# Performance work log

Hardware: AMD Instinct MI355X
Metric: run time of the kernel (lower is better)

The kernel has to match this reference:

```python
import jax, jax.numpy as jnp
import numpy as np
from jax import lax

N, C, H, W, Q, HD = 2, 64, 96, 96, 147456, 128

def make_coord(h, w):
    # pixel-center coords in [-1,1]; channel 0 -> H dim, channel 1 -> W dim
    y = -1.0 + (2.0 * jnp.arange(h) + 1.0) / h
    x = -1.0 + (2.0 * jnp.arange(w) + 1.0) / w
    yy, xx = jnp.meshgrid(y, x, indexing='ij')
    return jnp.stack([yy, xx], 0)[None]  # [1,2,h,w]

def _pix(c, n):
    # align_corners=False unnormalization
    return ((c + 1.0) * n - 1.0) / 2.0

def gather_nearest(img, cy, cx):
    # img [n,c,h,w]; cy,cx [n,q] in [-1,1] -> [n,q,c]
    n, c, h, w = img.shape
    iy = jnp.clip(jnp.round(_pix(cy, h)).astype(jnp.int32), 0, h - 1)
    ix = jnp.clip(jnp.round(_pix(cx, w)).astype(jnp.int32), 0, w - 1)
    flat = img.reshape(n, c, h * w)
    out = jnp.take_along_axis(flat, (iy * w + ix)[:, None, :], axis=2)
    return out.transpose(0, 2, 1)

def sample_bilinear_border(img, cy, cx):
    # grid_sample bilinear, padding_mode='border', align_corners=False
    n, c, h, w = img.shape
    fy = jnp.clip(_pix(cy, h), 0.0, h - 1.0)
    fx = jnp.clip(_pix(cx, w), 0.0, w - 1.0)
    y0 = jnp.floor(fy); x0 = jnp.floor(fx)
    wy = fy - y0; wx = fx - x0
    y0i = jnp.clip(y0.astype(jnp.int32), 0, h - 1); y1i = jnp.clip(y0i + 1, 0, h - 1)
    x0i = jnp.clip(x0.astype(jnp.int32), 0, w - 1); x1i = jnp.clip(x0i + 1, 0, w - 1)
    flat = img.reshape(n, c, h * w)
    def g(iy, ix):
        return jnp.take_along_axis(flat, (iy * w + ix)[:, None, :], axis=2)
    v = (g(y0i, x0i) * ((1 - wy) * (1 - wx))[:, None, :]
         + g(y0i, x1i) * ((1 - wy) * wx)[:, None, :]
         + g(y1i, x0i) * (wy * (1 - wx))[:, None, :]
         + g(y1i, x1i) * (wy * wx)[:, None, :])
    return v.transpose(0, 2, 1)

def mlp3(x, w1, b1, w2, b2, w3, b3):
    hdd = jax.nn.relu(x @ w1 + b1)
    hdd = jax.nn.relu(hdd @ w2 + b2)
    return hdd @ w3 + b3

def posenc(rel, hd):
    # sinusoid PE: 2 coord dims x (sin,cos) x hd//4 octave bands -> hd feats
    f = (2.0 ** jnp.arange(hd // 4)) * jnp.pi
    ang = rel[..., None] * f  # [n,q,2,hd//4]
    n, q = rel.shape[:2]
    return jnp.concatenate([jnp.sin(ang), jnp.cos(ang)], -1).reshape(n, q, hd)

def reference(lr, feat, raw_disp, coord, cell, coef_w, coef_b, freq_w, freq_b, phase_w,
              im_w1, im_b1, im_w2, im_b2, im_w3, im_b3,
              dp_w1, dp_b1, dp_w2, dp_b2, dp_w3, dp_b3):
    n, c, h, w = feat.shape
    hd = coef_b.shape[0]
    conv = lambda x, wk, bk: lax.conv_general_dilated(
        x, wk, (1, 1), 'SAME', dimension_numbers=('NCHW', 'OIHW', 'NCHW')) + bk[None, :, None, None]
    coef = conv(feat, coef_w, coef_b)
    freq = conv(feat, freq_w, freq_b)
    scale = 2.0 / (cell + 1e-6)[:, 0, 1] / w  # [n]
    disp = raw_disp * scale[:, None, None, None]
    mean_d = jnp.mean(disp, (1, 2, 3), keepdims=True)
    std_d = jnp.std(disp, (1, 2, 3), keepdims=True, ddof=1) + 1e-6
    dnorm = (disp - mean_d) / std_d
    rx, ry = 1.0 / h, 1.0 / w  # 2/dim/2
    fcoord = jnp.broadcast_to(make_coord(h, w), (n, 2, h, w))
    hw = jnp.array([h, w], coord.dtype)
    phase = (cell * hw) @ phase_w  # [n,q,hd]
    preds, pdisps, areas = [], [], []
    for vx in (-1, 1):
        for vy in (-1, 1):
            cy = jnp.clip(coord[:, :, 0] + vx * rx + 1e-6, -1 + 1e-6, 1 - 1e-6)
            cx = jnp.clip(coord[:, :, 1] + vy * ry + 1e-6, -1 + 1e-6, 1 - 1e-6)
            q_disp = gather_nearest(dnorm, cy, cx)   # [n,q,1]
            q_inp = gather_nearest(feat, cy, cx)     # [n,q,c]
            q_coef = gather_nearest(coef, cy, cx)    # [n,q,hd]
            q_freq = gather_nearest(freq, cy, cx)    # [n,q,hd]
            q_coord = gather_nearest(fcoord, cy, cx) # [n,q,2]
            rel = (coord - q_coord) * hw
            coord_ff = posenc(rel, hd)
            pdisps.append(mlp3(jnp.concatenate([q_disp, q_inp, rel], -1),
                               dp_w1, dp_b1, dp_w2, dp_b2, dp_w3, dp_b3))
            qf = q_freq * coord_ff + phase
            preds.append(mlp3(q_coef * qf, im_w1, im_b1, im_w2, im_b2, im_w3, im_b3))
            areas.append(jnp.abs(rel[:, :, 0] * rel[:, :, 1]) + 1e-9)
    tot = areas[0] + areas[1] + areas[2] + areas[3]
    order = [3, 2, 1, 0]  # local-ensemble diagonal area swap
    ret = sum(preds[i] * (areas[order[i]] / tot)[..., None] for i in range(4))
    ret_d = sum(pdisps[i] * (areas[order[i]] / tot)[..., None] for i in range(4))
    cy, cx = coord[:, :, 0], coord[:, :, 1]
    rgb = ret + sample_bilinear_border(lr, cy, cx)
    out_disp = ret_d + sample_bilinear_border(disp, cy, cx)
    return jnp.concatenate([rgb, out_disp], -1)  # [n,q,4]

def setup_inputs() -> dict:
    key = jax.random.key(0)
    ks = jax.random.split(key, 16)
    s = 0.02
    return {
        'lr': jax.random.uniform(ks[0], (N, 3, H, W), jnp.float32),
        'feat': jax.random.normal(ks[1], (N, C, H, W), jnp.float32),
        'raw_disp': jax.random.normal(ks[2], (N, 1, H, W), jnp.float32),
        'coord': jax.random.uniform(ks[3], (N, Q, 2), jnp.float32) * 2.0 - 1.0,
        'cell': jnp.full((N, Q, 2), 2.0 / 384.0, jnp.float32),
        'coef_w': jax.random.normal(ks[4], (HD, C, 3, 3), jnp.float32) * s,
        'coef_b': jnp.zeros((HD,), jnp.float32),
        'freq_w': jax.random.normal(ks[5], (HD, C, 3, 3), jnp.float32) * s,
        'freq_b': jnp.zeros((HD,), jnp.float32),
        'phase_w': jax.random.normal(ks[6], (2, HD), jnp.float32) * s,
        'im_w1': jax.random.normal(ks[7], (HD, 256), jnp.float32) * s,
        'im_b1': jnp.zeros((256,), jnp.float32),
        'im_w2': jax.random.normal(ks[8], (256, 256), jnp.float32) * s,
        'im_b2': jnp.zeros((256,), jnp.float32),
        'im_w3': jax.random.normal(ks[9], (256, 3), jnp.float32) * s,
        'im_b3': jnp.zeros((3,), jnp.float32),
        'dp_w1': jax.random.normal(ks[10], (C + 3, 256), jnp.float32) * s,
        'dp_b1': jnp.zeros((256,), jnp.float32),
        'dp_w2': jax.random.normal(ks[11], (256, 256), jnp.float32) * s,
        'dp_b2': jnp.zeros((256,), jnp.float32),
        'dp_w3': jax.random.normal(ks[12], (256, 1), jnp.float32) * s,
        'dp_b3': jnp.zeros((1,), jnp.float32),
    }
```

## Files before the change

kernel.cpp:

```cpp
#include <hip/hip_runtime.h>

#define QTOT 147456

typedef __attribute__((ext_vector_type(8))) short bf16x8;
typedef __attribute__((ext_vector_type(8))) unsigned short u16x8;
typedef __attribute__((ext_vector_type(4))) float f32x4;

union V8 { u16x8 v; unsigned short us[8]; };

__device__ __forceinline__ unsigned short f2b(float f){
  unsigned int u = __float_as_uint(f);
  return (unsigned short)((u + 0x7fffu + ((u >> 16) & 1u)) >> 16);
}
__device__ __forceinline__ float b2f(unsigned short s){
  return __uint_as_float(((unsigned int)s) << 16);
}

#define OFF_STATS   0
#define OFF_FPAD    256
#define OFF_SAMP    (OFF_FPAD + 2458624)
#define OFF_DNORM   (OFF_SAMP + 589824)
#define OFF_COEFT   (OFF_DNORM + 73728)
#define OFF_FREQT   (OFF_COEFT + 4718592)
#define OFF_WIM1    (OFF_FREQT + 4718592)
#define OFF_WIM2    (OFF_WIM1 + 65536)
#define OFF_WIM3    (OFF_WIM2 + 131072)
#define OFF_WDP1    (OFF_WIM3 + 8192)
#define OFF_WDP2    (OFF_WDP1 + 49152)
#define OFF_WDP3    (OFF_WDP2 + 131072)
#define OFF_WCV     (OFF_WDP3 + 8192)

__global__ void kStats(const float* __restrict__ raw_disp, const float* __restrict__ cell,
                       float* __restrict__ stats){
  int n = blockIdx.x;
  float cellv = cell[((size_t)n*QTOT)*2 + 1];
  float scale = 2.0f/(cellv + 1e-6f)/96.0f;
  __shared__ double sd[256], sq[256];
  double s=0.0, s2=0.0;
  for(int i=threadIdx.x;i<9216;i+=256){
    float d = raw_disp[(size_t)n*9216 + i]*scale;
    double dd = (double)d; s += dd; s2 += dd*dd;
  }
  sd[threadIdx.x]=s; sq[threadIdx.x]=s2; __syncthreads();
  for(int o=128;o>0;o>>=1){
    if(threadIdx.x<o){ sd[threadIdx.x]+=sd[threadIdx.x+o]; sq[threadIdx.x]+=sq[threadIdx.x+o]; }
    __syncthreads();
  }
  if(threadIdx.x==0){
    double mean = sd[0]/9216.0;
    double var  = (sq[0] - sd[0]*sd[0]/9216.0)/9215.0;
    if(var < 0.0) var = 0.0;
    stats[n*2+0] = (float)mean;
    stats[n*2+1] = (float)sqrt(var) + 1e-6f;
  }
}

__global__ void kPackImgs(const float* __restrict__ feat, const float* __restrict__ lr,
                          const float* __restrict__ raw_disp, const float* __restrict__ cell,
                          const float* __restrict__ stats,
                          unsigned short* __restrict__ featPad, float* __restrict__ sampT,
                          float* __restrict__ dnormT){
  int i = blockIdx.x*256 + threadIdx.x;
  if(i >= 2*98*98) return;
  int n = i/(98*98); int remi = i%(98*98);
  int py = remi/98, px = remi%98;
  bool inter = (py>=1 && py<=96 && px>=1 && px<=96);
  int y = py-1, x = px-1;
  for(int cb=0;cb<8;cb++){
    V8 v;
    #pragma unroll
    for(int e=0;e<8;e++){
      int c = cb*8+e;
      float f = inter ? feat[(((size_t)n*64 + c)*96 + y)*96 + x] : 0.0f;
      v.us[e] = f2b(f);
    }
    *(u16x8*)(featPad + (size_t)i*64 + cb*8) = v.v;
  }
  if(inter){
    float cellv = cell[((size_t)n*QTOT)*2 + 1];
    float scale = 2.0f/(cellv + 1e-6f)/96.0f;
    float d = raw_disp[((size_t)n*96 + y)*96 + x]*scale;
    size_t p = (size_t)n*9216 + y*96 + x;
    float4 sv;
    sv.x = lr[(((size_t)n*3 + 0)*96 + y)*96 + x];
    sv.y = lr[(((size_t)n*3 + 1)*96 + y)*96 + x];
    sv.z = lr[(((size_t)n*3 + 2)*96 + y)*96 + x];
    sv.w = d;
    *(float4*)(sampT + p*4) = sv;
    dnormT[p] = (d - stats[n*2+0]) / stats[n*2+1];
  }
}

__device__ __forceinline__ void packKN(unsigned short* dst, const float* src,
                                       int K, int N, int Npad, int i){
  int j = i & 7; int tt = i >> 3;
  int col = tt % Npad; tt /= Npad;
  int qq = tt & 3; int kc = tt >> 2;
  int k = kc*32 + qq*8 + j;
  float v = (k < K && col < N) ? src[(size_t)k*N + col] : 0.0f;
  dst[i] = f2b(v);
}

__global__ void kPackW(const float* im_w1, const float* im_w2, const float* im_w3,
                       const float* dp_w1, const float* dp_w2, const float* dp_w3,
                       const float* coef_w, const float* freq_w,
                       unsigned short* wIm1, unsigned short* wIm2, unsigned short* wIm3,
                       unsigned short* wDp1, unsigned short* wDp2, unsigned short* wDp3,
                       unsigned short* wCv){
  int i = blockIdx.x*256 + threadIdx.x;
  if(i < 32768){ packKN(wIm1, im_w1, 128, 256, 256, i); return; } i -= 32768;
  if(i < 65536){ packKN(wIm2, im_w2, 256, 256, 256, i); return; } i -= 65536;
  if(i < 4096){  packKN(wIm3, im_w3, 256, 3, 16, i);    return; } i -= 4096;
  if(i < 24576){ packKN(wDp1, dp_w1, 67, 256, 256, i);  return; } i -= 24576;
  if(i < 65536){ packKN(wDp2, dp_w2, 256, 256, 256, i); return; } i -= 65536;
  if(i < 4096){  packKN(wDp3, dp_w3, 256, 1, 16, i);    return; } i -= 4096;
  if(i < 147456){
    int ii = i;
    int j = ii & 7; int tt = ii >> 3;
    int col = tt % 128; tt /= 128;
    int qq = tt & 3; tt >>= 2;
    int kc = tt & 1; tt >>= 1;
    int tap = tt % 9; int z = tt / 9;
    int k = kc*32 + qq*8 + j;
    const float* w = z ? freq_w : coef_w;
    wCv[i] = f2b(w[((size_t)col*64 + k)*9 + tap]);
  }
}

__global__ __launch_bounds__(512) void kConv(const unsigned short* __restrict__ featPad,
                                             const unsigned short* __restrict__ wCv,
                                             const float* __restrict__ coef_b,
                                             const float* __restrict__ freq_b,
                                             unsigned short* __restrict__ coefT,
                                             unsigned short* __restrict__ freqT){
  int bx = blockIdx.x;
  int y  = blockIdx.y;
  int nz = blockIdx.z; int n = nz >> 1, z = nz & 1;
  const unsigned short* wp = wCv + (size_t)z*73728;
  const float* bias = z ? freq_b : coef_b;
  unsigned short* dst = z ? freqT : coefT;
  int t = threadIdx.x, lane = t & 63, w = t >> 6;
  int x0 = bx*48;
  int colBase = w*16 + (lane & 15);
  int qq = lane >> 4;
  f32x4 acc[3] = {};
  #pragma unroll
  for(int tap=0;tap<9;tap++){
    int ky = tap/3, kx = tap%3;
    #pragma unroll
    for(int kc=0;kc<2;kc++){
      bf16x8 bfr = *(const bf16x8*)(wp + (((size_t)(tap*2 + kc)*4 + qq)*128 + colBase)*8);
      #pragma unroll
      for(int mt=0;mt<3;mt++){
        int pxi = x0 + mt*16 + (lane & 15) + kx;
        int pyi = y + ky;
        const unsigned short* ap = featPad + (((size_t)n*98 + pyi)*98 + pxi)*64 + kc*32 + qq*8;
        bf16x8 afr = *(const bf16x8*)ap;
        acc[mt] = __builtin_amdgcn_mfma_f32_16x16x32_bf16(afr, bfr, acc[mt], 0, 0, 0);
      }
    }
  }
  float bv = bias[colBase];
  #pragma unroll
  for(int mt=0;mt<3;mt++){
    #pragma unroll
    for(int j=0;j<4;j++){
      int px = x0 + mt*16 + (lane>>4)*4 + j;
      dst[((size_t)n*9216 + y*96 + px)*128 + colBase] = f2b(acc[mt][j] + bv);
    }
  }
}

#define H1B 0u
#define XB  16384u
#define H2B 16384u

__global__ __launch_bounds__(256, 4) void kMega(
    const float* __restrict__ coord, const float* __restrict__ cell,
    const float* __restrict__ phase_w,
    const float* __restrict__ im_b1, const float* __restrict__ im_b2, const float* __restrict__ im_b3,
    const float* __restrict__ dp_b1, const float* __restrict__ dp_b2, const float* __restrict__ dp_b3,
    const unsigned short* __restrict__ coefT, const unsigned short* __restrict__ freqT,
    const unsigned short* __restrict__ featPad, const float* __restrict__ dnormT,
    const float* __restrict__ sampT,
    const unsigned short* __restrict__ wIm1, const unsigned short* __restrict__ wIm2,
    const unsigned short* __restrict__ wIm3,
    const unsigned short* __restrict__ wDp1, const unsigned short* __restrict__ wDp2,
    const unsigned short* __restrict__ wDp3,
    float* __restrict__ out){
  __shared__ __align__(128) char smem[32768];
  __shared__ float sPhW[256];
  __shared__ int   sIy[32], sIx[32];
  __shared__ float sRelY[32], sRelX[32], sArea[32], sQd[32];
  __shared__ float sPredIm[128], sPredDp[32];

  const int b = blockIdx.x;
  const int n = b / 18432;
  const int q0 = (b % 18432) * 8;
  const int t = threadIdx.x;
  const int lane = t & 63;
  const int w = t >> 6;

  sPhW[t] = phase_w[t];
  if(t < 32){
    int r = t;
    int q = q0 + (r >> 2); int v = r & 3;
    float vx = (v & 2) ? 1.0f : -1.0f;
    float vy = (v & 1) ? 1.0f : -1.0f;
    size_t ci = ((size_t)n*QTOT + q)*2;
    float cyo = coord[ci], cxo = coord[ci+1];
    const float RX = 1.0f/96.0f;
    float lo = -1.0f + 1e-6f, hi = 1.0f - 1e-6f;
    float cy = fminf(fmaxf(cyo + vx*RX + 1e-6f, lo), hi);
    float cx = fminf(fmaxf(cxo + vy*RX + 1e-6f, lo), hi);
    float fpy = ((cy + 1.0f)*96.0f - 1.0f)*0.5f;
    float fpx = ((cx + 1.0f)*96.0f - 1.0f)*0.5f;
    int iy = (int)rintf(fpy); iy = iy < 0 ? 0 : (iy > 95 ? 95 : iy);
    int ix = (int)rintf(fpx); ix = ix < 0 ? 0 : (ix > 95 ? 95 : ix);
    float qcy = -1.0f + (2.0f*(float)iy + 1.0f)/96.0f;
    float qcx = -1.0f + (2.0f*(float)ix + 1.0f)/96.0f;
    float ry = (cyo - qcy)*96.0f;
    float rx = (cxo - qcx)*96.0f;
    sIy[r]=iy; sIx[r]=ix; sRelY[r]=ry; sRelX[r]=rx;
    sArea[r] = fabsf(ry*rx) + 1e-9f;
    sQd[r] = dnormT[(size_t)n*9216 + iy*96 + ix];
  }
  __syncthreads();

  {
    int r = t >> 3, h8 = t & 7;
    int q = q0 + (r >> 2);
    int c0 = h8 * 16;
    float rel = (c0 < 64) ? sRelY[r] : sRelX[r];
    bool isCos = (c0 & 32) != 0;
    float rp = rel * 3.14159265358979323846f;
    double rev = (double)rp * 0.15915494309189535;
    if(c0 & 16) rev *= 65536.0;
    size_t ci = ((size_t)n*QTOT + q)*2;
    float pc0 = cell[ci]   * 96.0f;
    float pc1 = cell[ci+1] * 96.0f;
    int pix = sIy[r]*96 + sIx[r];
    const unsigned short* cp = coefT + ((size_t)n*9216 + pix)*128 + c0;
    const unsigned short* fp = freqT + ((size_t)n*9216 + pix)*128 + c0;
    unsigned rowb = XB + (unsigned)r*256u;
    for(int it=0; it<2; ++it){
      V8 qc, qf, ov;
      qc.v = *(const u16x8*)(cp + it*8);
      qf.v = *(const u16x8*)(fp + it*8);
      #pragma unroll
      for(int e=0;e<8;++e){
        double fr = rev - floor(rev);
        float fv = (float)fr;
        float ff = isCos ? __builtin_amdgcn_cosf(fv) : __builtin_amdgcn_sinf(fv);
        rev += rev;
        int c = c0 + it*8 + e;
        float ph = pc0*sPhW[c] + pc1*sPhW[128 + c];
        float xv = b2f(qc.us[e]) * (b2f(qf.us[e])*ff + ph);
        ov.us[e] = f2b(xv);
      }
      int ch = h8*2 + it;
      *(u16x8*)(smem + rowb + ((unsigned)(ch ^ (r & 7)) << 4)) = ov.v;
    }
  }
  __syncthreads();

  auto layerT = [&](int nkc, unsigned aBase, int aSh, const unsigned short* wp,
                    const float* bias, unsigned oBase){
    const int wn = w;
    f32x4 acc[2][4] = {};
    for(int kc=0; kc<nkc; ++kc){
      int ch = kc*4 + (lane >> 4);
      bf16x8 af[2], wf[4];
      #pragma unroll
      for(int mt=0; mt<2; ++mt){
        int r = mt*16 + (lane & 15);
        af[mt] = *(const bf16x8*)(smem + aBase + ((unsigned)r << aSh)
                                  + ((unsigned)(ch ^ (r & 7)) << 4));
      }
      #pragma unroll
      for(int nt=0; nt<4; ++nt){
        int col = wn*64 + nt*16 + (lane & 15);
        wf[nt] = *(const bf16x8*)(wp + ((size_t)ch*256 + col)*8);
      }
      #pragma unroll
      for(int mt=0; mt<2; ++mt)
        #pragma unroll
        for(int nt=0; nt<4; ++nt)
          acc[mt][nt] = __builtin_amdgcn_mfma_f32_16x16x32_bf16(wf[nt], af[mt], acc[mt][nt], 0,0,0);
    }
    #pragma unroll
    for(int nt=0; nt<4; ++nt){
      int n0 = wn*64 + nt*16 + (lane>>4)*4;
      float4 bv = *(const float4*)(bias + n0);
      #pragma unroll
      for(int mt=0; mt<2; ++mt){
        int r = mt*16 + (lane & 15);
        float h0 = fmaxf(acc[mt][nt][0] + bv.x, 0.0f);
        float h1 = fmaxf(acc[mt][nt][1] + bv.y, 0.0f);
        float h2 = fmaxf(acc[mt][nt][2] + bv.z, 0.0f);
        float h3 = fmaxf(acc[mt][nt][3] + bv.w, 0.0f);
        uint2 pv;
        pv.x = (unsigned)f2b(h0) | ((unsigned)f2b(h1) << 16);
        pv.y = (unsigned)f2b(h2) | ((unsigned)f2b(h3) << 16);
        *(uint2*)(smem + oBase + (unsigned)r*512u
                  + ((unsigned)(((n0>>3) ^ (r & 7))) << 4)
                  + (unsigned)((n0 & 7) << 1)) = pv;
      }
    }
  };

  auto layerOut = [&](const unsigned short* wp, float b30, float b31, float b32, bool isIm){
    if(w < 2){
      int mt = w;
      f32x4 acc = {};
      for(int kc=0; kc<8; ++kc){
        int ch = kc*4 + (lane >> 4);
        int r = mt*16 + (lane & 15);
        bf16x8 a  = *(const bf16x8*)(smem + H2B + (unsigned)r*512u
                                     + ((unsigned)(ch ^ (r & 7)) << 4));
        bf16x8 bb = *(const bf16x8*)(wp + ((size_t)ch*16 + (lane & 15))*8);
        acc = __builtin_amdgcn_mfma_f32_16x16x32_bf16(bb, a, acc, 0,0,0);
      }
      if(lane < 16){
        int row = mt*16 + lane;
        if(isIm){
          sPredIm[row*4+0] = acc[0] + b30;
          sPredIm[row*4+1] = acc[1] + b31;
          sPredIm[row*4+2] = acc[2] + b32;
        } else {
          sPredDp[row] = acc[0] + b30;
        }
      }
    }
  };

  float ib0 = im_b3[0], ib1 = im_b3[1], ib2 = im_b3[2];
  float db0 = dp_b3[0];

  layerT(4, XB, 8, wIm1, im_b1, H1B);   __syncthreads();
  layerT(8, H1B, 9, wIm2, im_b2, H2B);  __syncthreads();
  layerOut(wIm3, ib0, ib1, ib2, true);  __syncthreads();

  {
    int r = t >> 3, sg = t & 7;
    int py = sIy[r] + 1, px = sIx[r] + 1;
    const unsigned short* fpr = featPad + (((size_t)n*98 + py)*98 + px)*64;
    unsigned rowb = XB + (unsigned)r*256u;
    float qd = sQd[r], ry = sRelY[r], rx = sRelX[r];
    for(int ch = sg; ch < 12; ch += 8){
      V8 ov;
      #pragma unroll
      for(int e=0;e<8;++e){
        int c = ch*8 + e;
        unsigned short bits;
        if(c == 0) bits = f2b(qd);
        else if(c <= 64) bits = fpr[c-1];
        else if(c == 65) bits = f2b(ry);
        else if(c == 66) bits = f2b(rx);
        else bits = 0;
        ov.us[e] = bits;
      }
      *(u16x8*)(smem + rowb + ((unsigned)(ch ^ (r & 7)) << 4)) = ov.v;
    }
  }
  __syncthreads();

  layerT(3, XB, 8, wDp1, dp_b1, H1B);   __syncthreads();
  layerT(8, H1B, 9, wDp2, dp_b2, H2B);  __syncthreads();
  layerOut(wDp3, db0, 0.0f, 0.0f, false); __syncthreads();

  if(t < 32){
    int ql = t >> 2, ch = t & 3;
    int rb = ql*4;
    float a0=sArea[rb], a1=sArea[rb+1], a2=sArea[rb+2], a3=sArea[rb+3];
    float tot = a0 + a1 + a2 + a3;
    float w0=a3/tot, w1=a2/tot, w2=a1/tot, w3=a0/tot;
    float ret;
    if(ch < 3)
      ret = sPredIm[(rb+0)*4+ch]*w0 + sPredIm[(rb+1)*4+ch]*w1
          + sPredIm[(rb+2)*4+ch]*w2 + sPredIm[(rb+3)*4+ch]*w3;
    else
      ret = sPredDp[rb+0]*w0 + sPredDp[rb+1]*w1 + sPredDp[rb+2]*w2 + sPredDp[rb+3]*w3;
    int q = q0 + ql;
    size_t ci = ((size_t)n*QTOT + q)*2;
    float cy = coord[ci], cx = coord[ci+1];
    float fy = fminf(fmaxf(((cy + 1.0f)*96.0f - 1.0f)*0.5f, 0.0f), 95.0f);
    float fx = fminf(fmaxf(((cx + 1.0f)*96.0f - 1.0f)*0.5f, 0.0f), 95.0f);
    float y0f = floorf(fy), x0f = floorf(fx);
    float wy = fy - y0f, wx = fx - x0f;
    int y0i = (int)y0f; int x0i = (int)x0f;
    int y1i = y0i + 1 > 95 ? 95 : y0i + 1;
    int x1i = x0i + 1 > 95 ? 95 : x0i + 1;
    const float* sp = sampT + (size_t)n*9216*4;
    float v00 = sp[((size_t)y0i*96 + x0i)*4 + ch];
    float v01 = sp[((size_t)y0i*96 + x1i)*4 + ch];
    float v10 = sp[((size_t)y1i*96 + x0i)*4 + ch];
    float v11 = sp[((size_t)y1i*96 + x1i)*4 + ch];
    float samp = v00*((1.0f-wy)*(1.0f-wx)) + v01*((1.0f-wy)*wx)
               + v10*(wy*(1.0f-wx)) + v11*(wy*wx);
    out[((size_t)n*QTOT + q)*4 + ch] = ret + samp;
  }
}

extern "C" void kernel_launch(void* const* d_in, const int* in_sizes, int n_in,
                              void* d_out, int out_size, void* d_ws, size_t ws_size,
                              hipStream_t stream){
  const float* lr       = (const float*)d_in[0];
  const float* feat     = (const float*)d_in[1];
  const float* raw_disp = (const float*)d_in[2];
  const float* coord    = (const float*)d_in[3];
  const float* cell     = (const float*)d_in[4];
  const float* coef_w   = (const float*)d_in[5];
  const float* coef_b   = (const float*)d_in[6];
  const float* freq_w   = (const float*)d_in[7];
  const float* freq_b   = (const float*)d_in[8];
  const float* phase_w  = (const float*)d_in[9];
  const float* im_w1    = (const float*)d_in[10];
  const float* im_b1    = (const float*)d_in[11];
  const float* im_w2    = (const float*)d_in[12];
  const float* im_b2    = (const float*)d_in[13];
  const float* im_w3    = (const float*)d_in[14];
  const float* im_b3    = (const float*)d_in[15];
  const float* dp_w1    = (const float*)d_in[16];
  const float* dp_b1    = (const float*)d_in[17];
  const float* dp_w2    = (const float*)d_in[18];
  const float* dp_b2    = (const float*)d_in[19];
  const float* dp_w3    = (const float*)d_in[20];
  const float* dp_b3    = (const float*)d_in[21];

  char* ws = (char*)d_ws;
  float* stats            = (float*)(ws + OFF_STATS);
  unsigned short* featPad = (unsigned short*)(ws + OFF_FPAD);
  float* sampT            = (float*)(ws + OFF_SAMP);
  float* dnormT           = (float*)(ws + OFF_DNORM);
  unsigned short* coefT   = (unsigned short*)(ws + OFF_COEFT);
  unsigned short* freqT   = (unsigned short*)(ws + OFF_FREQT);
  unsigned short* wIm1    = (unsigned short*)(ws + OFF_WIM1);
  unsigned short* wIm2    = (unsigned short*)(ws + OFF_WIM2);
  unsigned short* wIm3    = (unsigned short*)(ws + OFF_WIM3);
  unsigned short* wDp1    = (unsigned short*)(ws + OFF_WDP1);
  unsigned short* wDp2    = (unsigned short*)(ws + OFF_WDP2);
  unsigned short* wDp3    = (unsigned short*)(ws + OFF_WDP3);
  unsigned short* wCv     = (unsigned short*)(ws + OFF_WCV);
  float* out = (float*)d_out;

  kStats<<<2, 256, 0, stream>>>(raw_disp, cell, stats);
  kPackImgs<<<(2*98*98 + 255)/256, 256, 0, stream>>>(feat, lr, raw_disp, cell, stats,
                                                     featPad, sampT, dnormT);
  kPackW<<<(344064 + 255)/256, 256, 0, stream>>>(im_w1, im_w2, im_w3, dp_w1, dp_w2, dp_w3,
                                                 coef_w, freq_w,
                                                 wIm1, wIm2, wIm3, wDp1, wDp2, wDp3, wCv);
  kConv<<<dim3(2, 96, 4), 512, 0, stream>>>(featPad, wCv, coef_b, freq_b, coefT, freqT);

  kMega<<<36864, 256, 0, stream>>>(coord, cell, phase_w,
                                   im_b1, im_b2, im_b3, dp_b1, dp_b2, dp_b3,
                                   coefT, freqT, featPad, dnormT, sampT,
                                   wIm1, wIm2, wIm3, wDp1, wDp2, wDp3, out);
}
```

Measured before the change: 783.7 us.

## Feed depth MLP first layer directly from global features and speed up PE math

Permutes the dp_w1 rows so the 64 feature channels come first. The depth-MLP first layer then loads its A operand straight from featPad in global memory, and the extra scalars come from a small shared buffer, which removes the shared-memory staging pass and one barrier. The positional-encoding loop replaces repeated double-precision floor and doubling with 64-bit fixed-point phase doubling. It also uses a transposed float2 phase-weight table and packs bf16 conversions with v_cvt_pk_bf16_f32. Risks include small rounding differences in the sinusoid phases and bf16 conversion, and uncoalesced global loads feeding the MFMA.

```diff
diff --git a/kernel.cpp b/kernel.cpp
--- a/kernel.cpp
+++ b/kernel.cpp
@@ -14,6 +14,11 @@
 }
 __device__ __forceinline__ float b2f(unsigned short s){
   return __uint_as_float(((unsigned int)s) << 16);
+}
+__device__ __forceinline__ unsigned cvtpk(float lo, float hi){
+  unsigned r;
+  asm("v_cvt_pk_bf16_f32 %0, %1, %2" : "=v"(r) : "v"(lo), "v"(hi));
+  return r;
 }
 
 #define OFF_STATS   0
@@ -111,7 +116,16 @@
   if(i < 32768){ packKN(wIm1, im_w1, 128, 256, 256, i); return; } i -= 32768;
   if(i < 65536){ packKN(wIm2, im_w2, 256, 256, 256, i); return; } i -= 65536;
   if(i < 4096){  packKN(wIm3, im_w3, 256, 3, 16, i);    return; } i -= 4096;
-  if(i < 24576){ packKN(wDp1, dp_w1, 67, 256, 256, i);  return; } i -= 24576;
+  if(i < 24576){
+    int j = i & 7; int tt = i >> 3;
+    int col = tt % 256; tt /= 256;
+    int qq = tt & 3; int kc = tt >> 2;
+    int kn = kc*32 + qq*8 + j;
+    int ko = (kn < 64) ? kn + 1 : ((kn == 64) ? 0 : kn);
+    float v = (kn < 67) ? dp_w1[(size_t)ko*256 + col] : 0.0f;
+    wDp1[i] = f2b(v);
+    return;
+  } i -= 24576;
   if(i < 65536){ packKN(wDp2, dp_w2, 256, 256, 256, i); return; } i -= 65536;
   if(i < 4096){  packKN(wDp3, dp_w3, 256, 1, 16, i);    return; } i -= 4096;
   if(i < 147456){
@@ -189,9 +203,10 @@
     const unsigned short* __restrict__ wDp3,
     float* __restrict__ out){
   __shared__ __align__(128) char smem[32768];
-  __shared__ float sPhW[256];
-  __shared__ int   sIy[32], sIx[32];
-  __shared__ float sRelY[32], sRelX[32], sArea[32], sQd[32];
+  __shared__ float2 sPhW2[128];
+  __shared__ int   sIy[32], sIx[32], sFoff[32];
+  __shared__ float sRelY[32], sRelX[32], sArea[32], sPc0[32], sPc1[32];
+  __shared__ unsigned short sXs[32*8];
   __shared__ float sPredIm[128], sPredDp[32];
 
   const int b = blockIdx.x;
@@ -201,7 +216,9 @@
   const int lane = t & 63;
   const int w = t >> 6;
 
-  sPhW[t] = phase_w[t];
+  if(t < 128){
+    sPhW2[((t & 15) << 3) | (t >> 4)] = make_float2(phase_w[t], phase_w[128 + t]);
+  }
   if(t < 32){
     int r = t;
     int q = q0 + (r >> 2); int v = r & 3;
@@ -223,22 +240,29 @@
     float rx = (cxo - qcx)*96.0f;
     sIy[r]=iy; sIx[r]=ix; sRelY[r]=ry; sRelX[r]=rx;
     sArea[r] = fabsf(ry*rx) + 1e-9f;
-    sQd[r] = dnormT[(size_t)n*9216 + iy*96 + ix];
+    sFoff[r] = ((n*98 + iy + 1)*98 + (ix + 1))*64;
+    float2 cl = *(const float2*)(cell + ci);
+    sPc0[r] = cl.x * 96.0f; sPc1[r] = cl.y * 96.0f;
+    float qd = dnormT[(size_t)n*9216 + iy*96 + ix];
+    V8 xr;
+    #pragma unroll
+    for(int e=0;e<8;++e) xr.us[e] = 0;
+    xr.us[0] = f2b(qd); xr.us[1] = f2b(ry); xr.us[2] = f2b(rx);
+    *(u16x8*)(sXs + r*8) = xr.v;
   }
   __syncthreads();
 
   {
     int r = t >> 3, h8 = t & 7;
-    int q = q0 + (r >> 2);
     int c0 = h8 * 16;
     float rel = (c0 < 64) ? sRelY[r] : sRelX[r];
     bool isCos = (c0 & 32) != 0;
     float rp = rel * 3.14159265358979323846f;
-    double rev = (double)rp * 0.15915494309189535;
-    if(c0 & 16) rev *= 65536.0;
-    size_t ci = ((size_t)n*QTOT + q)*2;
-    float pc0 = cell[ci]   * 96.0f;
-    float pc1 = cell[ci+1] * 96.0f;
+    double rev0 = (double)rp * 0.15915494309189535;
+    double rf = rev0 - floor(rev0);
+    unsigned long long F = (unsigned long long)(rf * 18446744073709551616.0);
+    if(c0 & 16) F <<= 16;
+    float pc0 = sPc0[r], pc1 = sPc1[r];
     int pix = sIy[r]*96 + sIx[r];
     const unsigned short* cp = coefT + ((size_t)n*9216 + pix)*128 + c0;
     const unsigned short* fp = freqT + ((size_t)n*9216 + pix)*128 + c0;
@@ -247,17 +271,19 @@
       V8 qc, qf, ov;
       qc.v = *(const u16x8*)(cp + it*8);
       qf.v = *(const u16x8*)(fp + it*8);
+      float xv[8];
       #pragma unroll
       for(int e=0;e<8;++e){
-        double fr = rev - floor(rev);
-        float fv = (float)fr;
+        float fv = (float)(unsigned)(F >> 32) * 0x1p-32f;
         float ff = isCos ? __builtin_amdgcn_cosf(fv) : __builtin_amdgcn_sinf(fv);
-        rev += rev;
-        int c = c0 + it*8 + e;
-        float ph = pc0*sPhW[c] + pc1*sPhW[128 + c];
-        float xv = b2f(qc.us[e]) * (b2f(qf.us[e])*ff + ph);
-        ov.us[e] = f2b(xv);
-      }
+        F += F;
+        float2 pw = sPhW2[(it*8 + e)*8 + h8];
+        float ph = pc0*pw.x + pc1*pw.y;
+        xv[e] = b2f(qc.us[e]) * (b2f(qf.us[e])*ff + ph);
+      }
+      unsigned* ow = (unsigned*)&ov;
+      ow[0] = cvtpk(xv[0], xv[1]); ow[1] = cvtpk(xv[2], xv[3]);
+      ow[2] = cvtpk(xv[4], xv[5]); ow[3] = cvtpk(xv[6], xv[7]);
       int ch = h8*2 + it;
       *(u16x8*)(smem + rowb + ((unsigned)(ch ^ (r & 7)) << 4)) = ov.v;
     }
@@ -300,8 +326,60 @@
         float h2 = fmaxf(acc[mt][nt][2] + bv.z, 0.0f);
         float h3 = fmaxf(acc[mt][nt][3] + bv.w, 0.0f);
         uint2 pv;
-        pv.x = (unsigned)f2b(h0) | ((unsigned)f2b(h1) << 16);
-        pv.y = (unsigned)f2b(h2) | ((unsigned)f2b(h3) << 16);
+        pv.x = cvtpk(h0, h1);
+        pv.y = cvtpk(h2, h3);
+        *(uint2*)(smem + oBase + (unsigned)r*512u
+                  + ((unsigned)(((n0>>3) ^ (r & 7))) << 4)
+                  + (unsigned)((n0 & 7) << 1)) = pv;
+      }
+    }
+  };
+
+  auto layerDp1 = [&](const unsigned short* wp, const float* bias, unsigned oBase){
+    const int wn = w;
+    f32x4 acc[2][4] = {};
+    int fo0 = sFoff[lane & 15];
+    int fo1 = sFoff[16 + (lane & 15)];
+    #pragma unroll
+    for(int kc=0; kc<3; ++kc){
+      int ch = kc*4 + (lane >> 4);
+      bf16x8 af[2], wf[4];
+      if(kc < 2){
+        int csub = kc*32 + (lane >> 4)*8;
+        af[0] = *(const bf16x8*)(featPad + fo0 + csub);
+        af[1] = *(const bf16x8*)(featPad + fo1 + csub);
+      } else {
+        af[0] = bf16x8{}; af[1] = bf16x8{};
+        if((lane >> 4) == 0){
+          af[0] = *(const bf16x8*)(sXs + (lane & 15)*8);
+          af[1] = *(const bf16x8*)(sXs + (16 + (lane & 15))*8);
+        }
+      }
+      #pragma unroll
+      for(int nt=0; nt<4; ++nt){
+        int col = wn*64 + nt*16 + (lane & 15);
+        wf[nt] = *(const bf16x8*)(wp + ((size_t)ch*256 + col)*8);
+      }
+      #pragma unroll
+      for(int mt=0; mt<2; ++mt)
+        #pragma unroll
+        for(int nt=0; nt<4; ++nt)
+          acc[mt][nt] = __builtin_amdgcn_mfma_f32_16x16x32_bf16(wf[nt], af[mt], acc[mt][nt], 0,0,0);
+    }
+    #pragma unroll
+    for(int nt=0; nt<4; ++nt){
+      int n0 = wn*64 + nt*16 + (lane>>4)*4;
+      float4 bv = *(const float4*)(bias + n0);
+      #pragma unroll
+      for(int mt=0; mt<2; ++mt){
+        int r = mt*16 + (lane & 15);
+        float h0 = fmaxf(acc[mt][nt][0] + bv.x, 0.0f);
+        float h1 = fmaxf(acc[mt][nt][1] + bv.y, 0.0f);
+        float h2 = fmaxf(acc[mt][nt][2] + bv.z, 0.0f);
+        float h3 = fmaxf(acc[mt][nt][3] + bv.w, 0.0f);
+        uint2 pv;
+        pv.x = cvtpk(h0, h1);
+        pv.y = cvtpk(h2, h3);
         *(uint2*)(smem + oBase + (unsigned)r*512u
                   + ((unsigned)(((n0>>3) ^ (r & 7))) << 4)
                   + (unsigned)((n0 & 7) << 1)) = pv;
@@ -341,31 +419,7 @@
   layerT(8, H1B, 9, wIm2, im_b2, H2B);  __syncthreads();
   layerOut(wIm3, ib0, ib1, ib2, true);  __syncthreads();
 
-  {
-    int r = t >> 3, sg = t & 7;
-    int py = sIy[r] + 1, px = sIx[r] + 1;
-    const unsigned short* fpr = featPad + (((size_t)n*98 + py)*98 + px)*64;
-    unsigned rowb = XB + (unsigned)r*256u;
-    float qd = sQd[r], ry = sRelY[r], rx = sRelX[r];
-    for(int ch = sg; ch < 12; ch += 8){
-      V8 ov;
-      #pragma unroll
-      for(int e=0;e<8;++e){
-        int c = ch*8 + e;
-        unsigned short bits;
-        if(c == 0) bits = f2b(qd);
-        else if(c <= 64) bits = fpr[c-1];
-        else if(c == 65) bits = f2b(ry);
-        else if(c == 66) bits = f2b(rx);
-        else bits = 0;
-        ov.us[e] = bits;
-      }
-      *(u16x8*)(smem + rowb + ((unsigned)(ch ^ (r & 7)) << 4)) = ov.v;
-    }
-  }
-  __syncthreads();
-
-  layerT(3, XB, 8, wDp1, dp_b1, H1B);   __syncthreads();
+  layerDp1(wDp1, dp_b1, H1B);           __syncthreads();
   layerT(8, H1B, 9, wDp2, dp_b2, H2B);  __syncthreads();
   layerOut(wDp3, db0, 0.0f, 0.0f, false); __syncthreads();
 
```

New measurement: 730.8 us. -6.7%, faster.
